# Kernel optimization log

Hardware: AMD Instinct MI355X
Metric: run time of the kernel (lower is better)

The kernel has to match this reference:

```python
import jax, jax.numpy as jnp
import numpy as np

N = 100000
E = 1600000
IN_DIM = 128
HID = 128
OUT_DIM = 64
ORDER = 4


def setup_inputs() -> dict:
    key = jax.random.key(0)
    ks = jax.random.split(key, 10)
    x = jax.random.normal(ks[0], (N, IN_DIM), dtype=jnp.float32)
    edge_index = jax.random.randint(ks[1], (2, E), 0, N, dtype=jnp.int64)
    gen_edge_index = jax.random.randint(ks[2], (2, E), 0, N, dtype=jnp.int64)
    s = 1.0 / np.sqrt(IN_DIM)
    w_orig = jax.random.normal(ks[3], (ORDER + 1, IN_DIM, HID), dtype=jnp.float32) * s
    b_orig = jax.random.normal(ks[4], (ORDER + 1, HID), dtype=jnp.float32) * s
    w_aug = jax.random.normal(ks[5], (ORDER + 1, IN_DIM, HID), dtype=jnp.float32) * s
    b_aug = jax.random.normal(ks[6], (ORDER + 1, HID), dtype=jnp.float32) * s
    fusion_weight = jnp.ones((2,), dtype=jnp.float32)
    clf_w = jax.random.normal(ks[7], (HID, OUT_DIM), dtype=jnp.float32) / np.sqrt(HID)
    clf_b = jax.random.normal(ks[8], (OUT_DIM,), dtype=jnp.float32) / np.sqrt(HID)
    return {"x": x, "edge_index": edge_index, "gen_edge_index": gen_edge_index,
            "w_orig": w_orig, "b_orig": b_orig, "w_aug": w_aug, "b_aug": b_aug,
            "fusion_weight": fusion_weight, "clf_w": clf_w, "clf_b": clf_b}


def _beta_wavelet(x, edge_index, W, b, num_nodes):
    # add self loops
    loop = jnp.arange(num_nodes, dtype=edge_index.dtype)
    row = jnp.concatenate([edge_index[0], loop])
    col = jnp.concatenate([edge_index[1], loop])
    # symmetric normalization D^{-1/2} A D^{-1/2}
    deg = jax.ops.segment_sum(jnp.ones_like(col, dtype=x.dtype), col, num_segments=num_nodes)
    dinv = jnp.where(deg > 0, deg ** -0.5, 0.0)
    norm = dinv[row] * dinv[col]  # [E+N]
    out = x @ W[0] + b[0]
    Tx = x
    for i in range(1, ORDER + 1):
        msg = norm[:, None] * Tx[row]                      # gather + scale [E+N, D]
        Tx = jax.ops.segment_sum(msg, col, num_segments=num_nodes)  # scatter_add
        out = out + Tx @ W[i] + b[i]
    return jax.nn.relu(out)


def reference(x, edge_index, gen_edge_index, w_orig, b_orig, w_aug, b_aug, fusion_weight, clf_w, clf_b):
    num_nodes = x.shape[0]
    h_orig = _beta_wavelet(x, edge_index, w_orig, b_orig, num_nodes)
    h_aug = _beta_wavelet(x, gen_edge_index, w_aug, b_aug, num_nodes)
    w = jax.nn.softmax(fusion_weight)
    h_final = w[0] * h_orig + w[1] * h_aug
    return h_final @ clf_w + clf_b
```

## Files before the change

### kernel.cpp

```cpp
#include <hip/hip_runtime.h>

#define N_NODES 100000
#define NPAD    100096
#define NE      1600000
#define DIM     128
#define ODIM    64
#define NORDER  4
#define NB      391
#define PB_EDGES 16384
#define PB_BLKS  98

typedef _Float16 h8 __attribute__((ext_vector_type(8)));
typedef float f4 __attribute__((ext_vector_type(4)));

__device__ __forceinline__ float2 up2(unsigned p) {
    union { unsigned u; _Float16 h[2]; } c; c.u = p;
    return make_float2((float)c.h[0], (float)c.h[1]);
}
__device__ __forceinline__ unsigned pk2(float x, float y) {
    union { unsigned u; _Float16 h[2]; } c;
    c.h[0] = (_Float16)x; c.h[1] = (_Float16)y;
    return c.u;
}
__device__ __forceinline__ unsigned short f2hbits(float x) {
    union { _Float16 h; unsigned short s; } c;
    c.h = (_Float16)x;
    return c.s;
}
__device__ __forceinline__ float h2f(unsigned short s) {
    union { unsigned short u; _Float16 h; } c;
    c.u = s;
    return (float)c.h;
}
__device__ __forceinline__ void async_cp16(const void* g, void* l) {
    __builtin_amdgcn_global_load_lds((const __attribute__((address_space(1))) void*)g,
                                     (__attribute__((address_space(3))) void*)l, 16, 0, 0);
}

__global__ __launch_bounds__(256) void hist_edges(const int* __restrict__ e0,
                                                  const int* __restrict__ e1,
                                                  int* __restrict__ bhist) {
    __shared__ int lh[NB];
    int t = threadIdx.x;
    int g = blockIdx.x >= 782;
    int blk = g ? (blockIdx.x - 782) : blockIdx.x;
    const int* colp = (g ? e1 : e0) + NE;
    int* bh = bhist + g * NB;
    for (int i = t; i < NB; i += 256) lh[i] = 0;
    __syncthreads();
    int base = blk * 2048 + t;
#pragma unroll
    for (int j = 0; j < 8; ++j) {
        int e = base + j * 256;
        if (e < NE) atomicAdd(&lh[colp[e] >> 8], 1);
    }
    __syncthreads();
    for (int i = t; i < NB; i += 256) if (lh[i]) atomicAdd(&bh[i], lh[i]);
}

__global__ void wave_scan(const int* __restrict__ in,
                          int* __restrict__ oexcl,
                          int* __restrict__ ocur,
                          int n) {
    int wv = threadIdx.x >> 6, lane = threadIdx.x & 63;
    if (wv >= 2) return;
    const int* I = in + wv * n;
    int* O = oexcl + wv * (n + 1);
    int* C = ocur + wv * n;
    int carry = 0;
    for (int base = 0; base < n; base += 64) {
        int i = base + lane;
        int v = (i < n) ? I[i] : 0;
        int s = v;
#pragma unroll
        for (int off = 1; off < 64; off <<= 1) {
            int x = __shfl_up(s, off, 64);
            if (lane >= off) s += x;
        }
        int excl = carry + s - v;
        if (i < n) {
            O[i] = excl;
            C[i] = excl;
        }
        carry += __shfl(s, 63, 64);
    }
    if (lane == 0) O[n] = carry;
}

__global__ __launch_bounds__(1024) void part_edges(const int* __restrict__ e0,
                                                   const int* __restrict__ e1,
                                                   int* __restrict__ bcursor,
                                                   unsigned* __restrict__ pairs) {
    __shared__ int lh[NB];
    __shared__ int lpos[NB];
    int t = threadIdx.x;
    int g = blockIdx.x >= PB_BLKS;
    int blk = g ? (blockIdx.x - PB_BLKS) : blockIdx.x;
    const int* rowp = (g ? e1 : e0);
    const int* colp = rowp + NE;
    int* bc = bcursor + g * NB;
    unsigned* pr = pairs + (size_t)g * NE;
    for (int i = t; i < NB; i += 1024) lh[i] = 0;
    __syncthreads();
    int base = blk * PB_EDGES + t;
    int rank[16];
    short bk[16];
    unsigned char lcv[16];
#pragma unroll
    for (int j = 0; j < 16; ++j) {
        int e = base + j * 1024;
        rank[j] = -1;
        if (e < NE) {
            int c = colp[e];
            bk[j] = (short)(c >> 8);
            lcv[j] = (unsigned char)(c & 255);
            rank[j] = atomicAdd(&lh[c >> 8], 1);
        }
    }
    __syncthreads();
    for (int i = t; i < NB; i += 1024) {
        int n = lh[i];
        lpos[i] = n ? atomicAdd(&bc[i], n) : 0;
    }
    __syncthreads();
#pragma unroll
    for (int j = 0; j < 16; ++j) {
        int e = base + j * 1024;
        if (e < NE) {
            int b = bk[j];
            pr[lpos[b] + rank[j]] = ((unsigned)rowp[e] << 8) | lcv[j];
        }
    }
}

__global__ __launch_bounds__(256) void bucket_csr(const unsigned* __restrict__ pairs,
                                                  const int* __restrict__ boff,
                                                  int* __restrict__ ptrv,
                                                  float* __restrict__ dinv,
                                                  int* __restrict__ srcv) {
    __shared__ int lcnt[256];
    __shared__ int lbase[256];
    int t = threadIdx.x;
    int g = blockIdx.x >= NB;
    int b = g ? (blockIdx.x - NB) : blockIdx.x;
    const unsigned* pr = pairs + (size_t)g * NE;
    const int* bo = boff + g * (NB + 1);
    int* pv = ptrv + g * (N_NODES + 1);
    float* dv = dinv + g * N_NODES;
    int* sv = srcv + (size_t)g * NE;
    lcnt[t] = 0;
    __syncthreads();
    int s = bo[b], e = bo[b + 1];
    for (int i = s + t; i < e; i += 256)
        atomicAdd(&lcnt[pr[i] & 255u], 1);
    __syncthreads();
    int v = lcnt[t];
    lbase[t] = v;
    __syncthreads();
    for (int off = 1; off < 256; off <<= 1) {
        int x = (t >= off) ? lbase[t - off] : 0;
        __syncthreads();
        lbase[t] += x;
        __syncthreads();
    }
    int node = (b << 8) + t;
    int gbase = s + lbase[t] - v;
    lbase[t] = gbase;
    lcnt[t] = 0;
    if (node < N_NODES) {
        pv[node] = gbase;
        dv[node] = rsqrtf((float)(v + 1));
    }
    if (b == 0 && g == 0 && t == 0) ptrv[N_NODES] = NE;
    if (b == 0 && g == 1 && t == 0) ptrv[2 * N_NODES + 1] = NE;
    __syncthreads();
    for (int i = s + t; i < e; i += 256) {
        unsigned pk = pr[i];
        int lc = (int)(pk & 255u);
        int pos = lbase[lc] + atomicAdd(&lcnt[lc], 1);
        sv[pos] = (int)(pk >> 8);
    }
}

__global__ __launch_bounds__(256) void s0cast(const float* __restrict__ x,
                                              const float* __restrict__ dinv,
                                              unsigned* __restrict__ S0o,
                                              unsigned* __restrict__ S0a) {
    int idx = blockIdx.x * 256 + threadIdx.x;
    if (idx >= NPAD * 64) return;
    int m = idx >> 6, u = idx & 63;
    if (m < N_NODES) {
        int e = (m << 7) + u * 2;
        float a = x[e], b = x[e + 1];
        float d0 = dinv[m];
        float d1 = dinv[N_NODES + m];
        S0o[idx] = pk2(d0 * a, d0 * b);
        S0a[idx] = pk2(d1 * a, d1 * b);
    } else {
        S0o[idx] = 0u;
        S0a[idx] = 0u;
    }
}

__global__ __launch_bounds__(256) void wcast(const float* __restrict__ Wo,
                                             const float* __restrict__ Wa,
                                             const float* __restrict__ cw,
                                             unsigned short* __restrict__ Wt) {
    int idx = blockIdx.x * 256 + threadIdx.x;
    if (idx >= 2 * 5 * DIM * DIM + ODIM * DIM) return;
    if (idx < 2 * 5 * DIM * DIM) {
        int g   = idx / (5 * DIM * DIM);
        int rem = idx % (5 * DIM * DIM);
        int i   = rem / (DIM * DIM);
        int r2  = rem % (DIM * DIM);
        int k8  = r2 >> 10;
        int n   = (r2 >> 3) & 127;
        int k7  = r2 & 7;
        int k   = k8 * 8 + k7;
        const float* W = g ? Wa : Wo;
        Wt[idx] = f2hbits(W[(i * DIM + k) * DIM + n]);
    } else {
        int j = idx - 2 * 5 * DIM * DIM;
        int n = j >> 7, k = j & 127;
        Wt[idx] = f2hbits(cw[k * ODIM + n]);
    }
}

template<int SIN>
__global__ __launch_bounds__(256) void propagate(const unsigned* __restrict__ Tin,
                                                 unsigned* __restrict__ Tout,
                                                 const int* __restrict__ ptrv,
                                                 const int* __restrict__ srcv,
                                                 const float* __restrict__ dinv) {
    int gid  = blockIdx.x * 256 + threadIdx.x;
    int lane = threadIdx.x & 63;
    int v    = __builtin_amdgcn_readfirstlane(gid >> 6);
    if (v >= N_NODES) return;
    float dv = dinv[v];
    float2 self = up2(Tin[(size_t)v * SIN + lane]);
    float ax = self.x, ay = self.y;
    int beg = ptrv[v], end = ptrv[v + 1];
    for (int k = beg; k < end; k += 16) {
        int u[16];
#pragma unroll
        for (int j = 0; j < 16; ++j) {
            int e  = k + j;
            int su = srcv[e < NE ? e : (NE - 1)];
            u[j]   = (e < end) ? su : N_NODES;
        }
        unsigned tw[16];
#pragma unroll
        for (int j = 0; j < 16; ++j)
            tw[j] = Tin[(size_t)((unsigned)u[j] * SIN) + lane];
#pragma unroll
        for (int j = 0; j < 16; ++j) {
            float2 t = up2(tw[j]);
            ax += t.x; ay += t.y;
        }
    }
    float s2 = dv * dv;
    Tout[(size_t)v * 256 + lane] = pk2(s2 * ax, s2 * ay);
}

__global__ __launch_bounds__(256, 3) void gemmH0(
        const unsigned short* __restrict__ A0,
        const unsigned short* __restrict__ A,
        const unsigned short* __restrict__ Wt,
        const float* __restrict__ bO,
        const float* __restrict__ dinv,
        const float* __restrict__ fw,
        unsigned short* __restrict__ H0) {
    __shared__ unsigned short Bl[DIM * DIM];
    __shared__ float bsl[DIM];
    int t = threadIdx.x;
    int lane = t & 63, wv = t >> 6;
    int m0 = blockIdx.x * 128 + wv * 32;
    int l15 = lane & 15, q = lane >> 4;
    if (t < 128) {
        float s = 0.f;
        for (int i = 0; i <= NORDER; ++i) s += bO[i * DIM + t];
        bsl[t] = s;
    }
    float f0 = fw[0], f1 = fw[1];
    float mx = fmaxf(f0, f1);
    float e0 = expf(f0 - mx), e1 = expf(f1 - mx);
    float sw0 = e0 / (e0 + e1);

    f4 acc[2][8];
#pragma unroll
    for (int mt = 0; mt < 2; ++mt)
#pragma unroll
        for (int nt = 0; nt < 8; ++nt) acc[mt][nt] = (f4)(0.f);

#pragma unroll
    for (int i = 0; i < 5; ++i) {
        const unsigned short* WtI = Wt + (size_t)i * DIM * DIM;
        const unsigned short* Ai = (i == 0) ? A0 : (A + (size_t)(i - 1) * DIM);
        const int rs = (i == 0) ? DIM : 512;
        h8 af[2][4];
#pragma unroll
        for (int mt = 0; mt < 2; ++mt)
#pragma unroll
            for (int kc = 0; kc < 4; ++kc)
                af[mt][kc] = *(const h8*)(Ai + (size_t)(m0 + mt * 16 + l15) * rs
                                             + (kc * 4 + q) * 8);
#pragma unroll
        for (int c = 0; c < 8; ++c) {
            int ci = c * 4 + wv;
            async_cp16(WtI + ci * 512 + lane * 8, &Bl[ci * 512]);
        }
        __syncthreads();
#pragma unroll
        for (int kc = 0; kc < 4; ++kc) {
            int c = kc * 4 + q;
#pragma unroll
            for (int nt = 0; nt < 8; ++nt) {
                h8 bf = *(const h8*)&Bl[(size_t)(c * 128 + nt * 16 + l15) * 8];
                acc[0][nt] = __builtin_amdgcn_mfma_f32_16x16x32_f16(af[0][kc], bf, acc[0][nt], 0, 0, 0);
                acc[1][nt] = __builtin_amdgcn_mfma_f32_16x16x32_f16(af[1][kc], bf, acc[1][nt], 0, 0, 0);
            }
        }
        __syncthreads();
    }
#pragma unroll
    for (int mt = 0; mt < 2; ++mt) {
        float rd[4];
#pragma unroll
        for (int r = 0; r < 4; ++r) {
            int row = m0 + mt * 16 + q * 4 + r;
            rd[r] = 1.0f / dinv[row < N_NODES ? row : (N_NODES - 1)];
        }
#pragma unroll
        for (int nt = 0; nt < 8; ++nt) {
            float bsv = bsl[nt * 16 + l15];
#pragma unroll
            for (int r = 0; r < 4; ++r) {
                int row = m0 + mt * 16 + q * 4 + r;
                H0[(size_t)row * DIM + nt * 16 + l15] =
                    f2hbits(sw0 * fmaxf(rd[r] * acc[mt][nt][r] + bsv, 0.f));
            }
        }
    }
}

__global__ __launch_bounds__(256, 2) void gemm_fused2(
        const unsigned short* __restrict__ A0,
        const unsigned short* __restrict__ A,
        const unsigned short* __restrict__ Wt,
        const unsigned short* __restrict__ H0,
        const float* __restrict__ bA,
        const float* __restrict__ dinv,
        const float* __restrict__ fw,
        const unsigned short* __restrict__ clfWt,
        const float* __restrict__ clfB,
        float* __restrict__ out) {
    __shared__ unsigned short BlH[DIM * 132];
    __shared__ float bsl[DIM];
    unsigned short* Bl = BlH;
    unsigned short* Hl = BlH;
    int t = threadIdx.x;
    int lane = t & 63, wv = t >> 6;
    int m0 = blockIdx.x * 128 + wv * 32;
    int l15 = lane & 15, q = lane >> 4;
    if (t < 128) {
        float s = 0.f;
        for (int i = 0; i <= NORDER; ++i) s += bA[i * DIM + t];
        bsl[t] = s;
    }
    float f0 = fw[0], f1 = fw[1];
    float mx = fmaxf(f0, f1);
    float e0 = expf(f0 - mx), e1 = expf(f1 - mx);
    float sw1 = e1 / (e0 + e1);

    f4 acc[2][8];
#pragma unroll
    for (int mt = 0; mt < 2; ++mt)
#pragma unroll
        for (int nt = 0; nt < 8; ++nt) acc[mt][nt] = (f4)(0.f);

#pragma unroll
    for (int i = 0; i < 5; ++i) {
        const unsigned short* WtI = Wt + (size_t)i * DIM * DIM;
        const unsigned short* Ai = (i == 0) ? A0 : (A + (size_t)(i - 1) * DIM);
        const int rs = (i == 0) ? DIM : 512;
        h8 af[2][4];
#pragma unroll
        for (int mt = 0; mt < 2; ++mt)
#pragma unroll
            for (int kc = 0; kc < 4; ++kc)
                af[mt][kc] = *(const h8*)(Ai + (size_t)(m0 + mt * 16 + l15) * rs
                                             + (kc * 4 + q) * 8);
#pragma unroll
        for (int c = 0; c < 8; ++c) {
            int ci = c * 4 + wv;
            async_cp16(WtI + ci * 512 + lane * 8, &Bl[ci * 512]);
        }
        __syncthreads();
#pragma unroll
        for (int kc = 0; kc < 4; ++kc) {
            int c = kc * 4 + q;
#pragma unroll
            for (int nt = 0; nt < 8; ++nt) {
                h8 bf = *(const h8*)&Bl[(size_t)(c * 128 + nt * 16 + l15) * 8];
                acc[0][nt] = __builtin_amdgcn_mfma_f32_16x16x32_f16(af[0][kc], bf, acc[0][nt], 0, 0, 0);
                acc[1][nt] = __builtin_amdgcn_mfma_f32_16x16x32_f16(af[1][kc], bf, acc[1][nt], 0, 0, 0);
            }
        }
        __syncthreads();
    }

#pragma unroll
    for (int mt = 0; mt < 2; ++mt) {
        float rd[4];
#pragma unroll
        for (int r = 0; r < 4; ++r) {
            int row = m0 + mt * 16 + q * 4 + r;
            rd[r] = 1.0f / dinv[row < N_NODES ? row : (N_NODES - 1)];
        }
#pragma unroll
        for (int nt = 0; nt < 8; ++nt) {
            float bsv = bsl[nt * 16 + l15];
            int col = nt * 16 + l15;
#pragma unroll
            for (int r = 0; r < 4; ++r) {
                int lrow = wv * 32 + mt * 16 + q * 4 + r;
                int grow = m0 + mt * 16 + q * 4 + r;
                float h = sw1 * fmaxf(rd[r] * acc[mt][nt][r] + bsv, 0.f)
                        + h2f(H0[(size_t)grow * DIM + col]);
                Hl[lrow * 132 + col] = f2hbits(h);
            }
        }
    }
    __syncthreads();

    f4 o[2][4];
#pragma unroll
    for (int mt = 0; mt < 2; ++mt)
#pragma unroll
        for (int n2 = 0; n2 < 4; ++n2) o[mt][n2] = (f4)(0.f);
#pragma unroll
    for (int kc = 0; kc < 4; ++kc) {
        int c = kc * 4 + q;
        h8 ha[2];
#pragma unroll
        for (int mt = 0; mt < 2; ++mt)
            ha[mt] = *(const h8*)&Hl[(wv * 32 + mt * 16 + l15) * 132 + c * 8];
#pragma unroll
        for (int n2 = 0; n2 < 4; ++n2) {
            h8 bf = *(const h8*)&clfWt[(size_t)(n2 * 16 + l15) * DIM + c * 8];
            o[0][n2] = __builtin_amdgcn_mfma_f32_16x16x32_f16(ha[0], bf, o[0][n2], 0, 0, 0);
            o[1][n2] = __builtin_amdgcn_mfma_f32_16x16x32_f16(ha[1], bf, o[1][n2], 0, 0, 0);
        }
    }
#pragma unroll
    for (int mt = 0; mt < 2; ++mt)
#pragma unroll
        for (int n2 = 0; n2 < 4; ++n2) {
            int col = n2 * 16 + l15;
            float cbv = clfB[col];
#pragma unroll
            for (int r = 0; r < 4; ++r) {
                int row = m0 + mt * 16 + q * 4 + r;
                if (row < N_NODES) out[(size_t)row * ODIM + col] = o[mt][n2][r] + cbv;
            }
        }
}

extern "C" void kernel_launch(void* const* d_in, const int* in_sizes, int n_in,
                              void* d_out, int out_size, void* d_ws, size_t ws_size,
                              hipStream_t stream) {
    const float* x   = (const float*)d_in[0];
    const int*   ei  = (const int*)d_in[1];
    const int*   gi  = (const int*)d_in[2];
    const float* w_o = (const float*)d_in[3];
    const float* b_o = (const float*)d_in[4];
    const float* w_a = (const float*)d_in[5];
    const float* b_a = (const float*)d_in[6];
    const float* fw  = (const float*)d_in[7];
    const float* cw  = (const float*)d_in[8];
    const float* cb  = (const float*)d_in[9];
    float* out = (float*)d_out;

    char* p = (char*)d_ws;
    auto alloc = [&](size_t bytes) {
        void* r = (void*)p;
        p += (bytes + 255) & ~(size_t)255;
        return r;
    };
    unsigned* Tbig = (unsigned*)alloc((size_t)NPAD * 256 * 4);
    unsigned* S0o  = (unsigned*)alloc((size_t)NPAD * 64 * 4);
    unsigned* S0a  = (unsigned*)alloc((size_t)NPAD * 64 * 4);
    unsigned short* H0 = (unsigned short*)alloc((size_t)NPAD * DIM * 2);
    unsigned short* Wt = (unsigned short*)alloc(((size_t)2 * 5 * DIM * DIM + ODIM * DIM) * 2);
    float* dinv  = (float*)alloc((size_t)2 * N_NODES * 4);
    unsigned* pairs = (unsigned*)alloc((size_t)2 * NE * 4);
    int* csr_src = (int*)alloc((size_t)2 * NE * 4);
    int* csr_ptr = (int*)alloc((size_t)2 * (N_NODES + 1) * 4);
    int* bhist   = (int*)alloc((size_t)2 * NB * 4);
    int* boff    = (int*)alloc((size_t)2 * (NB + 1) * 4);
    int* bcursor = (int*)alloc((size_t)2 * NB * 4);

    const int gP  = (N_NODES * 64 + 255) / 256;
    const int gX  = (NPAD * 64 + 255) / 256;
    const int gW  = (2 * 5 * DIM * DIM + ODIM * DIM + 255) / 256;
    const int gM  = NPAD / 128;

    hipMemsetAsync(Tbig + (size_t)N_NODES * 256, 0,
                   (size_t)(NPAD - N_NODES) * 256 * 4, stream);
    hipMemsetAsync(bhist, 0, (size_t)2 * NB * 4, stream);

    wcast<<<gW, 256, 0, stream>>>(w_o, w_a, cw, Wt);

    hist_edges<<<2 * 782, 256, 0, stream>>>(ei, gi, bhist);
    wave_scan<<<1, 128, 0, stream>>>(bhist, boff, bcursor, NB);
    part_edges<<<2 * PB_BLKS, 1024, 0, stream>>>(ei, gi, bcursor, pairs);
    bucket_csr<<<2 * NB, 256, 0, stream>>>(pairs, boff, csr_ptr, dinv, csr_src);

    s0cast<<<gX, 256, 0, stream>>>(x, dinv, S0o, S0a);

    propagate<64><<<gP, 256, 0, stream>>>(S0o, Tbig, csr_ptr, csr_src, dinv);
    propagate<256><<<gP, 256, 0, stream>>>(Tbig, Tbig + 64, csr_ptr, csr_src, dinv);
    propagate<256><<<gP, 256, 0, stream>>>(Tbig + 64, Tbig + 128, csr_ptr, csr_src, dinv);
    propagate<256><<<gP, 256, 0, stream>>>(Tbig + 128, Tbig + 192, csr_ptr, csr_src, dinv);
    gemmH0<<<gM, 256, 0, stream>>>((const unsigned short*)S0o, (const unsigned short*)Tbig,
                                   Wt, b_o, dinv, fw, H0);

    {
        const int* pv = csr_ptr + (N_NODES + 1);
        const int* sv = csr_src + (size_t)NE;
        const float* dv = dinv + (size_t)N_NODES;
        propagate<64><<<gP, 256, 0, stream>>>(S0a, Tbig, pv, sv, dv);
        propagate<256><<<gP, 256, 0, stream>>>(Tbig, Tbig + 64, pv, sv, dv);
        propagate<256><<<gP, 256, 0, stream>>>(Tbig + 64, Tbig + 128, pv, sv, dv);
        propagate<256><<<gP, 256, 0, stream>>>(Tbig + 128, Tbig + 192, pv, sv, dv);
    }
    gemm_fused2<<<gM, 256, 0, stream>>>((const unsigned short*)S0a,
                                        (const unsigned short*)Tbig,
                                        Wt + (size_t)5 * DIM * DIM,
                                        H0, b_a, dinv + N_NODES, fw,
                                        Wt + (size_t)2 * 5 * DIM * DIM, cb, out);
}
```

Baseline: 783.4 us.

## Load GEMM weights directly from global and precompute bias sums and softmax

The two dense GEMM kernels no longer stage each weight slice into LDS with async copies and two barriers per order. Each wave now reads B fragments straight from global memory, relying on the cache, since every block reuses the same small weight matrices. Bias sums and the softmax fusion weights are computed once in the weight-cast kernel instead of in every GEMM block. gemm_fused2 also copies its H0 tile into LDS in a coalesced pass rather than doing strided global reads in the epilogue. In exchange, gemmH0's launch bound drops from 3 to 2 blocks per CU, and the B operand now depends on cache hit rates.

```diff
diff --git a/kernel.cpp b/kernel.cpp
--- a/kernel.cpp
+++ b/kernel.cpp
@@ -31,10 +31,6 @@
     union { unsigned short u; _Float16 h; } c;
     c.u = s;
     return (float)c.h;
-}
-__device__ __forceinline__ void async_cp16(const void* g, void* l) {
-    __builtin_amdgcn_global_load_lds((const __attribute__((address_space(1))) void*)g,
-                                     (__attribute__((address_space(3))) void*)l, 16, 0, 0);
 }
 
 __global__ __launch_bounds__(256) void hist_edges(const int* __restrict__ e0,
@@ -205,9 +201,31 @@
 __global__ __launch_bounds__(256) void wcast(const float* __restrict__ Wo,
                                              const float* __restrict__ Wa,
                                              const float* __restrict__ cw,
-                                             unsigned short* __restrict__ Wt) {
+                                             const float* __restrict__ bO,
+                                             const float* __restrict__ bA,
+                                             const float* __restrict__ fw,
+                                             unsigned short* __restrict__ Wt,
+                                             float* __restrict__ params) {
     int idx = blockIdx.x * 256 + threadIdx.x;
     if (idx >= 2 * 5 * DIM * DIM + ODIM * DIM) return;
+    if (idx < 258) {
+        if (idx < 2) {
+            float f0 = fw[0], f1 = fw[1];
+            float mx = fmaxf(f0, f1);
+            float e0 = expf(f0 - mx), e1 = expf(f1 - mx);
+            params[idx] = (idx == 0 ? e0 : e1) / (e0 + e1);
+        } else if (idx < 130) {
+            int n = idx - 2;
+            float s = 0.f;
+            for (int i = 0; i <= NORDER; ++i) s += bO[i * DIM + n];
+            params[idx] = s;
+        } else {
+            int n = idx - 130;
+            float s = 0.f;
+            for (int i = 0; i <= NORDER; ++i) s += bA[i * DIM + n];
+            params[idx] = s;
+        }
+    }
     if (idx < 2 * 5 * DIM * DIM) {
         int g   = idx / (5 * DIM * DIM);
         int rem = idx % (5 * DIM * DIM);
@@ -262,29 +280,21 @@
     Tout[(size_t)v * 256 + lane] = pk2(s2 * ax, s2 * ay);
 }
 
-__global__ __launch_bounds__(256, 3) void gemmH0(
+__global__ __launch_bounds__(256, 2) void gemmH0(
         const unsigned short* __restrict__ A0,
         const unsigned short* __restrict__ A,
         const unsigned short* __restrict__ Wt,
-        const float* __restrict__ bO,
+        const float* __restrict__ params,
         const float* __restrict__ dinv,
-        const float* __restrict__ fw,
         unsigned short* __restrict__ H0) {
-    __shared__ unsigned short Bl[DIM * DIM];
-    __shared__ float bsl[DIM];
     int t = threadIdx.x;
     int lane = t & 63, wv = t >> 6;
     int m0 = blockIdx.x * 128 + wv * 32;
     int l15 = lane & 15, q = lane >> 4;
-    if (t < 128) {
-        float s = 0.f;
-        for (int i = 0; i <= NORDER; ++i) s += bO[i * DIM + t];
-        bsl[t] = s;
-    }
-    float f0 = fw[0], f1 = fw[1];
-    float mx = fmaxf(f0, f1);
-    float e0 = expf(f0 - mx), e1 = expf(f1 - mx);
-    float sw0 = e0 / (e0 + e1);
+    float sw0 = params[0];
+    float bs[8];
+#pragma unroll
+    for (int nt = 0; nt < 8; ++nt) bs[nt] = params[2 + nt * 16 + l15];
 
     f4 acc[2][8];
 #pragma unroll
@@ -305,22 +315,15 @@
                 af[mt][kc] = *(const h8*)(Ai + (size_t)(m0 + mt * 16 + l15) * rs
                                              + (kc * 4 + q) * 8);
 #pragma unroll
-        for (int c = 0; c < 8; ++c) {
-            int ci = c * 4 + wv;
-            async_cp16(WtI + ci * 512 + lane * 8, &Bl[ci * 512]);
-        }
-        __syncthreads();
-#pragma unroll
         for (int kc = 0; kc < 4; ++kc) {
             int c = kc * 4 + q;
 #pragma unroll
             for (int nt = 0; nt < 8; ++nt) {
-                h8 bf = *(const h8*)&Bl[(size_t)(c * 128 + nt * 16 + l15) * 8];
+                h8 bf = *(const h8*)(WtI + (size_t)(c * 128 + nt * 16 + l15) * 8);
                 acc[0][nt] = __builtin_amdgcn_mfma_f32_16x16x32_f16(af[0][kc], bf, acc[0][nt], 0, 0, 0);
                 acc[1][nt] = __builtin_amdgcn_mfma_f32_16x16x32_f16(af[1][kc], bf, acc[1][nt], 0, 0, 0);
             }
         }
-        __syncthreads();
     }
 #pragma unroll
     for (int mt = 0; mt < 2; ++mt) {
@@ -332,12 +335,11 @@
         }
 #pragma unroll
         for (int nt = 0; nt < 8; ++nt) {
-            float bsv = bsl[nt * 16 + l15];
 #pragma unroll
             for (int r = 0; r < 4; ++r) {
                 int row = m0 + mt * 16 + q * 4 + r;
                 H0[(size_t)row * DIM + nt * 16 + l15] =
-                    f2hbits(sw0 * fmaxf(rd[r] * acc[mt][nt][r] + bsv, 0.f));
+                    f2hbits(sw0 * fmaxf(rd[r] * acc[mt][nt][r] + bs[nt], 0.f));
             }
         }
     }
@@ -348,29 +350,21 @@
         const unsigned short* __restrict__ A,
         const unsigned short* __restrict__ Wt,
         const unsigned short* __restrict__ H0,
-        const float* __restrict__ bA,
+        const float* __restrict__ params,
         const float* __restrict__ dinv,
-        const float* __restrict__ fw,
         const unsigned short* __restrict__ clfWt,
         const float* __restrict__ clfB,
         float* __restrict__ out) {
-    __shared__ unsigned short BlH[DIM * 132];
-    __shared__ float bsl[DIM];
-    unsigned short* Bl = BlH;
-    unsigned short* Hl = BlH;
+    __shared__ unsigned short Hl[DIM * 132];
     int t = threadIdx.x;
     int lane = t & 63, wv = t >> 6;
-    int m0 = blockIdx.x * 128 + wv * 32;
+    int mb = blockIdx.x * 128;
+    int m0 = mb + wv * 32;
     int l15 = lane & 15, q = lane >> 4;
-    if (t < 128) {
-        float s = 0.f;
-        for (int i = 0; i <= NORDER; ++i) s += bA[i * DIM + t];
-        bsl[t] = s;
-    }
-    float f0 = fw[0], f1 = fw[1];
-    float mx = fmaxf(f0, f1);
-    float e0 = expf(f0 - mx), e1 = expf(f1 - mx);
-    float sw1 = e1 / (e0 + e1);
+    float sw1 = params[1];
+    float bs[8];
+#pragma unroll
+    for (int nt = 0; nt < 8; ++nt) bs[nt] = params[130 + nt * 16 + l15];
 
     f4 acc[2][8];
 #pragma unroll
@@ -391,23 +385,25 @@
                 af[mt][kc] = *(const h8*)(Ai + (size_t)(m0 + mt * 16 + l15) * rs
                                              + (kc * 4 + q) * 8);
 #pragma unroll
-        for (int c = 0; c < 8; ++c) {
-            int ci = c * 4 + wv;
-            async_cp16(WtI + ci * 512 + lane * 8, &Bl[ci * 512]);
-        }
-        __syncthreads();
-#pragma unroll
         for (int kc = 0; kc < 4; ++kc) {
             int c = kc * 4 + q;
 #pragma unroll
             for (int nt = 0; nt < 8; ++nt) {
-                h8 bf = *(const h8*)&Bl[(size_t)(c * 128 + nt * 16 + l15) * 8];
+                h8 bf = *(const h8*)(WtI + (size_t)(c * 128 + nt * 16 + l15) * 8);
                 acc[0][nt] = __builtin_amdgcn_mfma_f32_16x16x32_f16(af[0][kc], bf, acc[0][nt], 0, 0, 0);
                 acc[1][nt] = __builtin_amdgcn_mfma_f32_16x16x32_f16(af[1][kc], bf, acc[1][nt], 0, 0, 0);
             }
         }
-        __syncthreads();
-    }
+    }
+
+#pragma unroll
+    for (int j = 0; j < 8; ++j) {
+        int chunk = t + j * 256;
+        int row = chunk >> 4, c8 = chunk & 15;
+        *(h8*)&Hl[row * 132 + c8 * 8] =
+            *(const h8*)&H0[(size_t)(mb + row) * DIM + c8 * 8];
+    }
+    __syncthreads();
 
 #pragma unroll
     for (int mt = 0; mt < 2; ++mt) {
@@ -419,14 +415,12 @@
         }
 #pragma unroll
         for (int nt = 0; nt < 8; ++nt) {
-            float bsv = bsl[nt * 16 + l15];
             int col = nt * 16 + l15;
 #pragma unroll
             for (int r = 0; r < 4; ++r) {
                 int lrow = wv * 32 + mt * 16 + q * 4 + r;
-                int grow = m0 + mt * 16 + q * 4 + r;
-                float h = sw1 * fmaxf(rd[r] * acc[mt][nt][r] + bsv, 0.f)
-                        + h2f(H0[(size_t)grow * DIM + col]);
+                float h = sw1 * fmaxf(rd[r] * acc[mt][nt][r] + bs[nt], 0.f)
+                        + h2f(Hl[lrow * 132 + col]);
                 Hl[lrow * 132 + col] = f2hbits(h);
             }
         }
@@ -492,6 +486,7 @@
     unsigned* S0a  = (unsigned*)alloc((size_t)NPAD * 64 * 4);
     unsigned short* H0 = (unsigned short*)alloc((size_t)NPAD * DIM * 2);
     unsigned short* Wt = (unsigned short*)alloc(((size_t)2 * 5 * DIM * DIM + ODIM * DIM) * 2);
+    float* params = (float*)alloc(258 * 4);
     float* dinv  = (float*)alloc((size_t)2 * N_NODES * 4);
     unsigned* pairs = (unsigned*)alloc((size_t)2 * NE * 4);
     int* csr_src = (int*)alloc((size_t)2 * NE * 4);
@@ -509,7 +504,7 @@
                    (size_t)(NPAD - N_NODES) * 256 * 4, stream);
     hipMemsetAsync(bhist, 0, (size_t)2 * NB * 4, stream);
 
-    wcast<<<gW, 256, 0, stream>>>(w_o, w_a, cw, Wt);
+    wcast<<<gW, 256, 0, stream>>>(w_o, w_a, cw, b_o, b_a, fw, Wt, params);
 
     hist_edges<<<2 * 782, 256, 0, stream>>>(ei, gi, bhist);
     wave_scan<<<1, 128, 0, stream>>>(bhist, boff, bcursor, NB);
@@ -523,7 +518,7 @@
     propagate<256><<<gP, 256, 0, stream>>>(Tbig + 64, Tbig + 128, csr_ptr, csr_src, dinv);
     propagate<256><<<gP, 256, 0, stream>>>(Tbig + 128, Tbig + 192, csr_ptr, csr_src, dinv);
     gemmH0<<<gM, 256, 0, stream>>>((const unsigned short*)S0o, (const unsigned short*)Tbig,
-                                   Wt, b_o, dinv, fw, H0);
+                                   Wt, params, dinv, H0);
 
     {
         const int* pv = csr_ptr + (N_NODES + 1);
@@ -537,6 +532,6 @@
     gemm_fused2<<<gM, 256, 0, stream>>>((const unsigned short*)S0a,
                                         (const unsigned short*)Tbig,
                                         Wt + (size_t)5 * DIM * DIM,
-                                        H0, b_a, dinv + N_NODES, fw,
+                                        H0, params, dinv + N_NODES,
                                         Wt + (size_t)2 * 5 * DIM * DIM, cb, out);
 }
```

Result: slower. 899.8 us (+14.9%).
